# Kernel tuning notes

Measured on AMD Instinct MI355X. Metric: run time of the kernel, lower is better.

The kernel has to match this reference:

```python
import jax, jax.numpy as jnp
import numpy as np

EPS = 1e-5
NUM_HEADS = 8

def _inorm(x):
    # InstanceNorm1d (affine=False): normalize over last (length) axis per (B, C)
    m = x.mean(axis=-1, keepdims=True)
    v = x.var(axis=-1, keepdims=True)  # biased variance, as torch instance norm
    return (x - m) * jax.lax.rsqrt(v + EPS)

def setup_inputs() -> dict:
    key = jax.random.key(0)
    ks = jax.random.split(key, 12)
    B, Nl, HW = 4, 1024, 4096
    Cl, Cv, Ck, Cval, Cout = 512, 512, 256, 256, 256
    w = lambda k, shape: (jax.random.normal(k, shape, jnp.float32) * 0.02)
    return {
        "l": jax.random.normal(ks[0], (B, Nl, Cl), jnp.float32),
        "x": jax.random.normal(ks[1], (B, HW, Cv), jnp.float32),
        "Wq": w(ks[2], (Ck, Cl)),   "bq": w(ks[3], (Ck,)),
        "Wk": w(ks[4], (Ck, Cv)),   "bk": w(ks[5], (Ck,)),
        "Wv": w(ks[6], (Cval, Cv)), "bv": w(ks[7], (Cval,)),
        "Ww": w(ks[8], (Cout, Cval)), "bw": w(ks[9], (Cout,)),
    }

def reference(l, x, Wq, bq, Wk, bk, Wv, bv, Ww, bw):
    H = NUM_HEADS
    Ck = Wq.shape[0]
    Cv = Wv.shape[0]
    dk, dv = Ck // H, Cv // H
    B, Nl, _ = l.shape
    HW = x.shape[1]

    # 1x1 Conv1d == per-position linear
    q = jnp.einsum('blc,kc->blk', l, Wq) + bq                     # [B, Nl, Ck]
    k = jnp.einsum('bnc,kc->bkn', x, Wk) + bk[None, :, None]      # [B, Ck, HW]
    k = _inorm(k)                                                  # InstanceNorm over HW
    v = jnp.einsum('bnc,kc->bkn', x, Wv) + bv[None, :, None]      # [B, Cv, HW]

    q = q.reshape(B, Nl, H, dk).transpose(0, 2, 1, 3)             # [B, H, Nl, dk]
    k = k.reshape(B, H, dk, HW)                                   # [B, H, dk, HW]
    v = v.reshape(B, H, dv, HW)                                   # [B, H, dv, HW]

    sim = jnp.einsum('bhld,bhdn->bhln', q, k) * (Ck ** -0.5)      # [B, H, Nl, HW]
    att = jax.nn.softmax(sim, axis=-1)
    out = jnp.einsum('bhln,bhdn->bhld', att, v)                   # [B, H, Nl, dv]

    out = out.transpose(0, 2, 1, 3).reshape(B, Nl, Cv)            # [B, Nl, Cv]
    out = jnp.einsum('blc,oc->bol', out, Ww) + bw[None, :, None]  # [B, Cout, Nl]
    out = _inorm(out)                                              # InstanceNorm over Nl
    return out.transpose(0, 2, 1)                                  # [B, Nl, Cout]
```

## Files before the change

### kernel.cpp

```cpp
#include <hip/hip_runtime.h>

constexpr int Bn = 4, NL = 1024, HWn = 4096, NH = 8;

typedef __attribute__((ext_vector_type(8))) short bf16x8;
typedef __attribute__((ext_vector_type(4))) float f32x4;
#define MFMA16 __builtin_amdgcn_mfma_f32_16x16x32_bf16

extern "C" __device__ float __ocml_native_exp2_f32(float);

__device__ __forceinline__ float b2f(unsigned short u) {
  union { unsigned int i; float f; } x; x.i = ((unsigned int)u) << 16; return x.f;
}
__device__ __forceinline__ unsigned short f2b(float f) {
  union { float f; unsigned int i; } x; x.f = f;
  unsigned int r = x.i + 0x7fffu + ((x.i >> 16) & 1u);
  return (unsigned short)(r >> 16);
}

__device__ __forceinline__ void async_load16(const unsigned short* g, unsigned short* l) {
  __builtin_amdgcn_global_load_lds(
      (const __attribute__((address_space(1))) unsigned int*)g,
      (__attribute__((address_space(3))) unsigned int*)l, 16, 0, 0);
}

__global__ __launch_bounds__(256) void convall(const float* __restrict__ x,
    const float* __restrict__ l,
    const float* __restrict__ Wk, const float* __restrict__ Wv,
    const float* __restrict__ Wq, const float* __restrict__ Ww,
    unsigned short* __restrict__ xbf, unsigned short* __restrict__ lbf,
    unsigned short* __restrict__ wkb, unsigned short* __restrict__ wvb,
    unsigned short* __restrict__ wqb,
    unsigned short* __restrict__ wwh, unsigned short* __restrict__ wwl,
    float* __restrict__ Fz)
{
  const int id = blockIdx.x, tid = threadIdx.x;
  if (id < 8192) {
    int i = (id * 256 + tid) * 4;
    float4 v = *(const float4*)(x + i);
    ushort4 o; o.x = f2b(v.x); o.y = f2b(v.y); o.z = f2b(v.z); o.w = f2b(v.w);
    *(ushort4*)(xbf + i) = o;
  } else if (id < 10240) {
    int i = ((id - 8192) * 256 + tid) * 4;
    float4 v = *(const float4*)(l + i);
    ushort4 o; o.x = f2b(v.x); o.y = f2b(v.y); o.z = f2b(v.z); o.w = f2b(v.w);
    *(ushort4*)(lbf + i) = o;
  } else if (id < 10752) {
    int sub = id - 10240;
    int y = sub >> 7, bx = sub & 127;
    int i = (bx * 256 + tid) * 4;
    if (y == 3) {
      if (i >= 65536) return;
      float4 v = *(const float4*)(Ww + i);
      ushort4 hi, lo;
      hi.x = f2b(v.x); lo.x = f2b(v.x - b2f(hi.x));
      hi.y = f2b(v.y); lo.y = f2b(v.y - b2f(hi.y));
      hi.z = f2b(v.z); lo.z = f2b(v.z - b2f(hi.z));
      hi.w = f2b(v.w); lo.w = f2b(v.w - b2f(hi.w));
      *(ushort4*)(wwh + i) = hi;
      *(ushort4*)(wwl + i) = lo;
      return;
    }
    const float* src = y == 0 ? Wk : (y == 1 ? Wv : Wq);
    unsigned short* dst = y == 0 ? wkb : (y == 1 ? wvb : wqb);
    float4 v = *(const float4*)(src + i);
    ushort4 o; o.x = f2b(v.x); o.y = f2b(v.y); o.z = f2b(v.z); o.w = f2b(v.w);
    *(ushort4*)(dst + i) = o;
  } else {
    int i = (id - 10752) * 1024 + tid * 4;
    *(float4*)(Fz + i) = (float4){0.f, 0.f, 0.f, 0.f};
  }
}

__global__ __launch_bounds__(256, 3) void gemm128(
    const unsigned short* __restrict__ xbf, const unsigned short* __restrict__ lbf,
    const unsigned short* __restrict__ wkb, const unsigned short* __restrict__ wvb,
    const unsigned short* __restrict__ wqb,
    const float* __restrict__ bk, const float* __restrict__ bv, const float* __restrict__ bq,
    unsigned short* __restrict__ khb, unsigned short* __restrict__ vfrag,
    unsigned short* __restrict__ qbuf,
    float* __restrict__ ksum, float* __restrict__ kss, float* __restrict__ vcs)
{
  __shared__ unsigned short As[2][4096];
  __shared__ unsigned short Bs[2][4096];
  const int id = blockIdx.x;
  const int mode = id < 256 ? 0 : (id < 512 ? 1 : 2);
  const int local = id - (mode == 0 ? 0 : (mode == 1 ? 256 : 512));
  const int rb = local >> 1, cb = local & 1;
  const int m0 = rb * 128, n0 = cb * 128;
  const unsigned short* A = (mode == 2) ? lbf : xbf;
  const unsigned short* W = (mode == 0) ? wkb : (mode == 1 ? wvb : wqb);
  const float* bias = (mode == 0) ? bk : (mode == 1 ? bv : bq);

  const int tid = threadIdx.x, w = tid >> 6, lane = tid & 63;
  const int quad = lane >> 4, l15 = lane & 15;
  const int wr = w >> 1, wc = w & 1;

  const int p0 = tid, p1 = tid + 256;
  const int am0 = p0 >> 2, ak0 = (p0 & 3) * 8;
  const int am1 = p1 >> 2, ak1 = (p1 & 3) * 8;

  f32x4 acc[4][4];
#pragma unroll
  for (int i = 0; i < 4; ++i)
#pragma unroll
    for (int j = 0; j < 4; ++j) acc[i][j] = (f32x4){0.f, 0.f, 0.f, 0.f};

  async_load16(A + (size_t)(m0 + am0) * 512 + ak0, &As[0][p0 * 8]);
  async_load16(A + (size_t)(m0 + am1) * 512 + ak1, &As[0][p1 * 8]);
  async_load16(W + (size_t)(n0 + am0) * 512 + ak0, &Bs[0][p0 * 8]);
  async_load16(W + (size_t)(n0 + am1) * 512 + ak1, &Bs[0][p1 * 8]);

  for (int kt = 0; kt < 16; ++kt) {
    const int cur = kt & 1;
    __syncthreads();
    if (kt < 15) {
      int k0 = (kt + 1) * 32;
      async_load16(A + (size_t)(m0 + am0) * 512 + k0 + ak0, &As[cur ^ 1][p0 * 8]);
      async_load16(A + (size_t)(m0 + am1) * 512 + k0 + ak1, &As[cur ^ 1][p1 * 8]);
      async_load16(W + (size_t)(n0 + am0) * 512 + k0 + ak0, &Bs[cur ^ 1][p0 * 8]);
      async_load16(W + (size_t)(n0 + am1) * 512 + k0 + ak1, &Bs[cur ^ 1][p1 * 8]);
    }
    bf16x8 af[4], bf[4];
#pragma unroll
    for (int fr = 0; fr < 4; ++fr)
      af[fr] = *(const bf16x8*)&As[cur][(wr * 64 + fr * 16 + l15) * 32 + quad * 8];
#pragma unroll
    for (int fc = 0; fc < 4; ++fc)
      bf[fc] = *(const bf16x8*)&Bs[cur][(wc * 64 + fc * 16 + l15) * 32 + quad * 8];
#pragma unroll
    for (int fr = 0; fr < 4; ++fr)
#pragma unroll
      for (int fc = 0; fc < 4; ++fc)
        acc[fr][fc] = MFMA16(af[fr], bf[fc], acc[fr][fc], 0, 0, 0);
  }

  float bb[4];
#pragma unroll
  for (int fc = 0; fc < 4; ++fc) bb[fc] = bias[n0 + wc * 64 + fc * 16 + l15];

  if (mode != 2) {
    const int b = m0 >> 12;
    const int seg = (m0 & 4095) >> 9;
#pragma unroll
    for (int fc = 0; fc < 4; ++fc) {
      float s = 0.f, ssq = 0.f;
#pragma unroll
      for (int fr = 0; fr < 4; ++fr)
#pragma unroll
        for (int r = 0; r < 4; ++r) {
          float v = acc[fr][fc][r] + bb[fc];
          s += v; ssq += v * v;
        }
      s += __shfl_xor(s, 16); s += __shfl_xor(s, 32);
      if (mode == 0) {
        ssq += __shfl_xor(ssq, 16); ssq += __shfl_xor(ssq, 32);
        if (quad == 0) {
          int col = n0 + wc * 64 + fc * 16 + l15;
          atomicAdd(&ksum[b * 256 + col], s);
          atomicAdd(&kss[b * 256 + col], ssq);
        }
      } else if (quad == 0) {
        int col = n0 + wc * 64 + fc * 16 + l15;
        atomicAdd(&vcs[seg * 1024 + b * 256 + col], s);
      }
    }
  }

  if (mode == 1) {
    const int b = m0 >> 12;
    const int seg64 = ((m0 & 4095) >> 6) + wr;
#pragma unroll
    for (int fc = 0; fc < 4; ++fc) {
      int col = n0 + wc * 64 + fc * 16 + l15;
      int h = col >> 5, d = col & 31;
      int dvt = d >> 4, ll = d & 15;
      size_t base = (size_t)((b * 8 + h) * 64 + seg64) * 2048 + dvt * 512;
#pragma unroll
      for (int fr = 0; fr < 4; ++fr) {
#pragma unroll
        for (int r = 0; r < 4; ++r) {
          int kappa = 4 * (quad * 4 + r) + fr;
          int kh2 = kappa >> 5, lq = (kappa >> 3) & 3, j = kappa & 7;
          vfrag[base + kh2 * 1024 + (lq * 16 + ll) * 8 + j] = f2b(acc[fr][fc][r] + bb[fc]);
        }
      }
    }
  } else {
    unsigned short* dst = (mode == 0) ? khb : qbuf;
#pragma unroll
    for (int fr = 0; fr < 4; ++fr) {
#pragma unroll
      for (int fc = 0; fc < 4; ++fc) {
        int col = n0 + wc * 64 + fc * 16 + l15;
#pragma unroll
        for (int r = 0; r < 4; ++r) {
          int row = m0 + wr * 64 + fr * 16 + quad * 4 + r;
          unsigned short val = f2b(acc[fr][fc][r] + bb[fc]);
          if (mode == 2) {
            dst[(size_t)row * 256 + col] = val;
          } else {
            int b = row >> 12, n = row & 4095, h = col >> 5, d = col & 31;
            dst[((size_t)(b * 8 + h) * 4096 + n) * 32 + d] = val;
          }
        }
      }
    }
  }
}

__global__ __launch_bounds__(256, 4) void attn10(const unsigned short* __restrict__ qbuf,
    const unsigned short* __restrict__ khb, const unsigned short* __restrict__ vfrag,
    const float* __restrict__ ksum, const float* __restrict__ kss,
    const float* __restrict__ vcs,
    float* __restrict__ po, float* __restrict__ pd)
{
  const int bh = blockIdx.x, b = bh >> 3, h = bh & 7;
  const int lsuper = blockIdx.y, quarter = blockIdx.z;
  const int tid = threadIdx.x, w = tid >> 6, lane = tid & 63;
  const int quad = lane >> 4, l15 = lane & 15;

  __shared__ unsigned short ps[4][2][16][64];

  bf16x8 qa[2];
  {
    float fold[8];
    const int ch = bh * 32 + quad * 8;
#pragma unroll
    for (int j = 0; j < 8; ++j) {
      float m = ksum[ch + j] * (1.f / 4096.f);
      float var = kss[ch + j] * (1.f / 4096.f) - m * m;
      fold[j] = rsqrtf(var + 1e-5f) * (0.0625f * 1.44269504f);
    }
#pragma unroll
    for (int lf = 0; lf < 2; ++lf) {
      int l = lsuper * 128 + w * 32 + lf * 16 + l15;
      bf16x8 qr = *(const bf16x8*)(qbuf + ((size_t)(b * NL + l)) * 256 + h * 32 + quad * 8);
      const unsigned short* qq = (const unsigned short*)&qr;
      unsigned short tmp[8];
#pragma unroll
      for (int j = 0; j < 8; ++j) tmp[j] = f2b(b2f(qq[j]) * fold[j]);
      qa[lf] = *(const bf16x8*)tmp;
    }
  }

  float drow[2][4];
  f32x4 acc[2][2];
#pragma unroll
  for (int lf = 0; lf < 2; ++lf) {
#pragma unroll
    for (int r = 0; r < 4; ++r) drow[lf][r] = 0.f;
    acc[lf][0] = (f32x4){0.f,0.f,0.f,0.f};
    acc[lf][1] = (f32x4){0.f,0.f,0.f,0.f};
  }

  const unsigned short* kl = khb + (size_t)bh * 131072 + (size_t)quarter * 32768
                             + l15 * 32 + quad * 8;
  const unsigned short* vl = vfrag + (size_t)bh * 131072 + (size_t)quarter * 32768
                             + lane * 8;

  unsigned short* psw = &ps[w][0][0][0];
  const unsigned rdswz = (unsigned)((l15 & 7) << 4);

  for (int c = 0; c < 16; ++c) {
    bf16x8 kb[4], vb[4];
#pragma unroll
    for (int t = 0; t < 4; ++t)
      kb[t] = *(const bf16x8*)(kl + c * 2048 + t * 512);
#pragma unroll
    for (int i = 0; i < 4; ++i)
      vb[i] = *(const bf16x8*)(vl + c * 2048 + i * 512);

    const f32x4 z = (f32x4){0.f,0.f,0.f,0.f};
#pragma unroll
    for (int lf = 0; lf < 2; ++lf) {
      f32x4 sv[4];
      __builtin_amdgcn_s_setprio(1);
#pragma unroll
      for (int t = 0; t < 4; ++t) sv[t] = MFMA16(qa[lf], kb[t], z, 0, 0, 0);
      __builtin_amdgcn_s_setprio(0);
#pragma unroll
      for (int r = 0; r < 4; ++r) {
        float x0 = __ocml_native_exp2_f32(sv[0][r]);
        float x1 = __ocml_native_exp2_f32(sv[1][r]);
        float x2 = __ocml_native_exp2_f32(sv[2][r]);
        float x3 = __ocml_native_exp2_f32(sv[3][r]);
        drow[lf][r] += (x0 + x1) + (x2 + x3);
        unsigned pk0, pk1;
        asm("v_cvt_pk_bf16_f32 %0, %1, %2" : "=v"(pk0) : "v"(x0 - 1.0f), "v"(x1 - 1.0f));
        asm("v_cvt_pk_bf16_f32 %0, %1, %2" : "=v"(pk1) : "v"(x2 - 1.0f), "v"(x3 - 1.0f));
        const int row = quad * 4 + r;
        unsigned off = (unsigned)((l15 * 8) ^ ((row & 7) << 4));
        uint2 pk; pk.x = pk0; pk.y = pk1;
        *(uint2*)((char*)(psw + lf * 1024 + row * 64) + off) = pk;
      }
      asm volatile("s_waitcnt lgkmcnt(0)" ::: "memory");
      __builtin_amdgcn_s_setprio(1);
#pragma unroll
      for (int kh2 = 0; kh2 < 2; ++kh2) {
        unsigned off = (unsigned)((kh2 * 64 + quad * 16) ^ rdswz);
        bf16x8 pa = *(const bf16x8*)((const char*)(psw + lf * 1024 + l15 * 64) + off);
        acc[lf][0] = MFMA16(pa, vb[kh2 * 2 + 0], acc[lf][0], 0, 0, 0);
        acc[lf][1] = MFMA16(pa, vb[kh2 * 2 + 1], acc[lf][1], 0, 0, 0);
      }
      __builtin_amdgcn_s_setprio(0);
    }
  }

  const float* vc0 = vcs + (quarter * 2) * 1024 + bh * 32;
  const float* vc1 = vc0 + 1024;
  float cs0 = vc0[l15] + vc1[l15];
  float cs1 = vc0[16 + l15] + vc1[16 + l15];
#pragma unroll
  for (int lf = 0; lf < 2; ++lf)
#pragma unroll
    for (int r = 0; r < 4; ++r) {
      acc[lf][0][r] += cs0;
      acc[lf][1][r] += cs1;
    }

  const size_t PDo = (size_t)quarter * 32768 + (size_t)bh * 1024;
#pragma unroll
  for (int lf = 0; lf < 2; ++lf) {
#pragma unroll
    for (int r = 0; r < 4; ++r) {
      float sv = drow[lf][r];
      sv += __shfl_xor(sv, 1, 16);
      sv += __shfl_xor(sv, 2, 16);
      sv += __shfl_xor(sv, 4, 16);
      sv += __shfl_xor(sv, 8, 16);
      int l = lsuper * 128 + w * 32 + lf * 16 + quad * 4 + r;
      float2 val; val.x = acc[lf][0][r]; val.y = acc[lf][1][r];
      *(float2*)(po + (PDo + l) * 32 + l15 * 2) = val;
      if (l15 == 0) pd[PDo + l] = sv;
    }
  }
}

__global__ __launch_bounds__(256) void combine4(const float* __restrict__ po,
    const float* __restrict__ pd, unsigned short* __restrict__ aoh,
    unsigned short* __restrict__ aol)
{
  int gid = blockIdx.x * 256 + threadIdx.x;
  int dv = gid & 31, l = (gid >> 5) & (NL - 1), h = (gid >> 15) & 7, b = gid >> 18;
  int c = ((dv & 15) << 1) | (dv >> 4);
  size_t r = ((size_t)(b * 8 + h)) * 1024 + l;
  float d = 0.f, o = 0.f;
#pragma unroll
  for (int q = 0; q < 4; ++q) {
    size_t rr = (size_t)q * 32768 + r;
    d += pd[rr];
    o += po[rr * 32 + c];
  }
  o = o / d;
  unsigned short hi = f2b(o);
  size_t idx = ((size_t)(b * NL) + l) * 256 + h * 32 + dv;
  aoh[idx] = hi;
  aol[idx] = f2b(o - b2f(hi));
}

__global__ __launch_bounds__(256) void gemm_proj(
    const unsigned short* __restrict__ aoh, const unsigned short* __restrict__ aol,
    const unsigned short* __restrict__ wwh, const unsigned short* __restrict__ wwl,
    const float* __restrict__ bw, float* __restrict__ pj,
    float* __restrict__ psum, float* __restrict__ psq)
{
  __shared__ unsigned short As[64 * 32];
  __shared__ unsigned short Bs[64 * 32];
  const int bm = blockIdx.x * 64, bn = blockIdx.y * 64;
  const int tid = threadIdx.x, w = tid >> 6, lane = tid & 63;
  const int quad = lane >> 4, l15 = lane & 15;
  const int wr = w >> 1, wc = w & 1;
  const int arow = tid >> 2, apiece = (tid & 3) * 8;

  f32x4 acc[2][2];
#pragma unroll
  for (int i = 0; i < 2; ++i)
#pragma unroll
    for (int j = 0; j < 2; ++j) acc[i][j] = (f32x4){0.f, 0.f, 0.f, 0.f};

  for (int pair = 0; pair < 3; ++pair) {
    const unsigned short* A = (pair == 1) ? aol : aoh;
    const unsigned short* Bm = (pair == 2) ? wwl : wwh;
    for (int kt = 0; kt < 8; ++kt) {
      int k0 = kt * 32;
      __syncthreads();
      *(bf16x8*)&As[tid * 8] = *(const bf16x8*)(A + (size_t)(bm + arow) * 256 + k0 + apiece);
      *(bf16x8*)&Bs[tid * 8] = *(const bf16x8*)(Bm + (size_t)(bn + arow) * 256 + k0 + apiece);
      __syncthreads();
      bf16x8 af[2], bf[2];
#pragma unroll
      for (int fr = 0; fr < 2; ++fr)
        af[fr] = *(const bf16x8*)&As[(wr * 32 + fr * 16 + l15) * 32 + quad * 8];
#pragma unroll
      for (int fc = 0; fc < 2; ++fc)
        bf[fc] = *(const bf16x8*)&Bs[(wc * 32 + fc * 16 + l15) * 32 + quad * 8];
#pragma unroll
      for (int fr = 0; fr < 2; ++fr)
#pragma unroll
        for (int fc = 0; fc < 2; ++fc)
          acc[fr][fc] = MFMA16(af[fr], bf[fc], acc[fr][fc], 0, 0, 0);
    }
  }

  const int b = bm >> 10;
#pragma unroll
  for (int fr = 0; fr < 2; ++fr)
#pragma unroll
    for (int fc = 0; fc < 2; ++fc) {
      int col = bn + wc * 32 + fc * 16 + l15;
      float bb = bw[col];
      float s = 0.f, ssq = 0.f;
#pragma unroll
      for (int r = 0; r < 4; ++r) {
        int row = bm + wr * 32 + fr * 16 + quad * 4 + r;
        float v = acc[fr][fc][r] + bb;
        pj[(size_t)row * 256 + col] = v;
        s += v; ssq += v * v;
      }
      s += __shfl_xor(s, 16); s += __shfl_xor(s, 32);
      ssq += __shfl_xor(ssq, 16); ssq += __shfl_xor(ssq, 32);
      if (quad == 0) {
        atomicAdd(&psum[b * 256 + col], s);
        atomicAdd(&psq[b * 256 + col], ssq);
      }
    }
}

__global__ __launch_bounds__(256) void final_out(const float* __restrict__ proj,
    const float* __restrict__ psum, const float* __restrict__ psq,
    float* __restrict__ out)
{
  const int b = blockIdx.x, o = threadIdx.x;
  const int l1 = blockIdx.y * 16;
  const float m = psum[b * 256 + o] * (1.f / 1024.f);
  const float r = rsqrtf(psq[b * 256 + o] * (1.f / 1024.f) - m * m + 1e-5f);
  for (int i = 0; i < 16; ++i) {
    size_t idx = ((size_t)(b * NL + l1 + i)) * 256 + o;
    out[idx] = (proj[idx] - m) * r;
  }
}

extern "C" void kernel_launch(void* const* d_in, const int* in_sizes, int n_in,
                              void* d_out, int out_size, void* d_ws, size_t ws_size,
                              hipStream_t stream)
{
  const float* l  = (const float*)d_in[0];
  const float* x  = (const float*)d_in[1];
  const float* Wq = (const float*)d_in[2];
  const float* bq = (const float*)d_in[3];
  const float* Wk = (const float*)d_in[4];
  const float* bk = (const float*)d_in[5];
  const float* Wv = (const float*)d_in[6];
  const float* bv = (const float*)d_in[7];
  const float* Ww = (const float*)d_in[8];
  const float* bw = (const float*)d_in[9];
  float* out = (float*)d_out;

  unsigned short* up = (unsigned short*)d_ws;
  unsigned short* xbf   = up;
  unsigned short* lbf   = xbf   + 8388608;
  unsigned short* wkb   = lbf   + 2097152;
  unsigned short* wvb   = wkb   + 131072;
  unsigned short* wqb   = wvb   + 131072;
  unsigned short* qbuf  = wqb   + 131072;
  unsigned short* khb   = qbuf  + 1048576;
  unsigned short* vhb   = khb   + 4194304;
  unsigned short* vfrag = vhb   + 4194304;
  unsigned short* aoh   = vfrag + 4194304;
  unsigned short* aol   = aoh   + 1048576;
  unsigned short* wwh   = aol   + 1048576;
  unsigned short* wwl   = wwh   + 65536;
  float* F     = (float*)((char*)d_ws + 53477376);
  float* ksum  = F;
  float* kss   = F + 1024;
  float* vcs   = F + 2048;
  float* psum  = F + 10240;
  float* psq   = F + 11264;
  float* po    = F + 15360;
  float* pd    = po + 4194304;
  float* pj    = po;

  dim3 blk(256);
  convall<<<10764, blk, 0, stream>>>(x, l, Wk, Wv, Wq, Ww, xbf, lbf,
                                     wkb, wvb, wqb, wwh, wwl, F);
  gemm128<<<576, blk, 0, stream>>>(xbf, lbf, wkb, wvb, wqb, bk, bv, bq,
                                   khb, vfrag, qbuf, ksum, kss, vcs);
  attn10<<<dim3(32, 8, 4), blk, 0, stream>>>(qbuf, khb, vfrag, ksum, kss, vcs, po, pd);
  combine4<<<4096, blk, 0, stream>>>(po, pd, aoh, aol);
  gemm_proj<<<dim3(64, 4), blk, 0, stream>>>(aoh, aol, wwh, wwl, bw, pj, psum, psq);
  final_out<<<dim3(4, 64), blk, 0, stream>>>(pj, psum, psq, out);
}
```

Measured before the change: 172.6 us.

## Fuse attention split-K combine into attention kernel, stage V-fragment stores, pipeline proj GEMM

The attention kernel no longer splits the HW axis into four quarters. Each block now walks all 64 key chunks for 16 query rows per wave and normalizes its output in place, writing the hi/lo bf16 split directly. This removes the combine4 kernel and the round trip of partial outputs and denominators through global memory, at the cost of fewer query rows per wave and a smaller grid. Separately, the QKV GEMM stages its V-fragment output through LDS so global stores become 16-byte coalesced, and the projection GEMM gains double-buffered async LDS loads.

```diff
diff --git a/kernel.cpp b/kernel.cpp
--- a/kernel.cpp
+++ b/kernel.cpp
@@ -80,8 +80,9 @@
     unsigned short* __restrict__ qbuf,
     float* __restrict__ ksum, float* __restrict__ kss, float* __restrict__ vcs)
 {
-  __shared__ unsigned short As[2][4096];
-  __shared__ unsigned short Bs[2][4096];
+  __shared__ unsigned short sh[16384];
+  unsigned short* As0 = sh;
+  unsigned short* Bs0 = sh + 8192;
   const int id = blockIdx.x;
   const int mode = id < 256 ? 0 : (id < 512 ? 1 : 2);
   const int local = id - (mode == 0 ? 0 : (mode == 1 ? 256 : 512));
@@ -105,28 +106,29 @@
 #pragma unroll
     for (int j = 0; j < 4; ++j) acc[i][j] = (f32x4){0.f, 0.f, 0.f, 0.f};
 
-  async_load16(A + (size_t)(m0 + am0) * 512 + ak0, &As[0][p0 * 8]);
-  async_load16(A + (size_t)(m0 + am1) * 512 + ak1, &As[0][p1 * 8]);
-  async_load16(W + (size_t)(n0 + am0) * 512 + ak0, &Bs[0][p0 * 8]);
-  async_load16(W + (size_t)(n0 + am1) * 512 + ak1, &Bs[0][p1 * 8]);
+  async_load16(A + (size_t)(m0 + am0) * 512 + ak0, &As0[p0 * 8]);
+  async_load16(A + (size_t)(m0 + am1) * 512 + ak1, &As0[p1 * 8]);
+  async_load16(W + (size_t)(n0 + am0) * 512 + ak0, &Bs0[p0 * 8]);
+  async_load16(W + (size_t)(n0 + am1) * 512 + ak1, &Bs0[p1 * 8]);
 
   for (int kt = 0; kt < 16; ++kt) {
     const int cur = kt & 1;
     __syncthreads();
     if (kt < 15) {
       int k0 = (kt + 1) * 32;
-      async_load16(A + (size_t)(m0 + am0) * 512 + k0 + ak0, &As[cur ^ 1][p0 * 8]);
-      async_load16(A + (size_t)(m0 + am1) * 512 + k0 + ak1, &As[cur ^ 1][p1 * 8]);
-      async_load16(W + (size_t)(n0 + am0) * 512 + k0 + ak0, &Bs[cur ^ 1][p0 * 8]);
-      async_load16(W + (size_t)(n0 + am1) * 512 + k0 + ak1, &Bs[cur ^ 1][p1 * 8]);
+      int nx = (cur ^ 1) * 4096;
+      async_load16(A + (size_t)(m0 + am0) * 512 + k0 + ak0, &As0[nx + p0 * 8]);
+      async_load16(A + (size_t)(m0 + am1) * 512 + k0 + ak1, &As0[nx + p1 * 8]);
+      async_load16(W + (size_t)(n0 + am0) * 512 + k0 + ak0, &Bs0[nx + p0 * 8]);
+      async_load16(W + (size_t)(n0 + am1) * 512 + k0 + ak1, &Bs0[nx + p1 * 8]);
     }
     bf16x8 af[4], bf[4];
 #pragma unroll
     for (int fr = 0; fr < 4; ++fr)
-      af[fr] = *(const bf16x8*)&As[cur][(wr * 64 + fr * 16 + l15) * 32 + quad * 8];
+      af[fr] = *(const bf16x8*)&As0[cur * 4096 + (wr * 64 + fr * 16 + l15) * 32 + quad * 8];
 #pragma unroll
     for (int fc = 0; fc < 4; ++fc)
-      bf[fc] = *(const bf16x8*)&Bs[cur][(wc * 64 + fc * 16 + l15) * 32 + quad * 8];
+      bf[fc] = *(const bf16x8*)&Bs0[cur * 4096 + (wc * 64 + fc * 16 + l15) * 32 + quad * 8];
 #pragma unroll
     for (int fr = 0; fr < 4; ++fr)
 #pragma unroll
@@ -167,23 +169,31 @@
   }
 
   if (mode == 1) {
-    const int b = m0 >> 12;
-    const int seg64 = ((m0 & 4095) >> 6) + wr;
+    __syncthreads();
 #pragma unroll
     for (int fc = 0; fc < 4; ++fc) {
-      int col = n0 + wc * 64 + fc * 16 + l15;
-      int h = col >> 5, d = col & 31;
-      int dvt = d >> 4, ll = d & 15;
-      size_t base = (size_t)((b * 8 + h) * 64 + seg64) * 2048 + dvt * 512;
+      const int ls = wr * 4 + wc * 2 + ((fc * 16 + l15) >> 5);
+      const int dvt = fc & 1;
 #pragma unroll
       for (int fr = 0; fr < 4; ++fr) {
 #pragma unroll
         for (int r = 0; r < 4; ++r) {
           int kappa = 4 * (quad * 4 + r) + fr;
           int kh2 = kappa >> 5, lq = (kappa >> 3) & 3, j = kappa & 7;
-          vfrag[base + kh2 * 1024 + (lq * 16 + ll) * 8 + j] = f2b(acc[fr][fc][r] + bb[fc]);
+          sh[ls * 2048 + kh2 * 1024 + dvt * 512 + lq * 128 + l15 * 8 + j] =
+              f2b(acc[fr][fc][r] + bb[fc]);
         }
       }
+    }
+    __syncthreads();
+    const int b2 = m0 >> 12, h0 = cb * 4, seg64b = (m0 & 4095) >> 6;
+#pragma unroll
+    for (int i = 0; i < 8; ++i) {
+      int p = i * 256 + tid;
+      int ls = p >> 8, off8 = (p & 255) * 8;
+      int dh = ls & 3, wr2 = ls >> 2;
+      size_t dst = ((size_t)((b2 * 8 + h0 + dh) * 64) + seg64b + wr2) * 2048 + off8;
+      *(bf16x8*)(vfrag + dst) = *(const bf16x8*)&sh[ls * 2048 + off8];
     }
   } else {
     unsigned short* dst = (mode == 0) ? khb : qbuf;
@@ -208,20 +218,20 @@
   }
 }
 
-__global__ __launch_bounds__(256, 4) void attn10(const unsigned short* __restrict__ qbuf,
+__global__ __launch_bounds__(256, 2) void attn11(const unsigned short* __restrict__ qbuf,
     const unsigned short* __restrict__ khb, const unsigned short* __restrict__ vfrag,
     const float* __restrict__ ksum, const float* __restrict__ kss,
     const float* __restrict__ vcs,
-    float* __restrict__ po, float* __restrict__ pd)
+    unsigned short* __restrict__ aoh, unsigned short* __restrict__ aol)
 {
   const int bh = blockIdx.x, b = bh >> 3, h = bh & 7;
-  const int lsuper = blockIdx.y, quarter = blockIdx.z;
+  const int lsuper = blockIdx.y;
   const int tid = threadIdx.x, w = tid >> 6, lane = tid & 63;
   const int quad = lane >> 4, l15 = lane & 15;
 
-  __shared__ unsigned short ps[4][2][16][64];
-
-  bf16x8 qa[2];
+  __shared__ unsigned short ps[4][16][64];
+
+  bf16x8 qa;
   {
     float fold[8];
     const int ch = bh * 32 + quad * 8;
@@ -231,37 +241,27 @@
       float var = kss[ch + j] * (1.f / 4096.f) - m * m;
       fold[j] = rsqrtf(var + 1e-5f) * (0.0625f * 1.44269504f);
     }
-#pragma unroll
-    for (int lf = 0; lf < 2; ++lf) {
-      int l = lsuper * 128 + w * 32 + lf * 16 + l15;
-      bf16x8 qr = *(const bf16x8*)(qbuf + ((size_t)(b * NL + l)) * 256 + h * 32 + quad * 8);
-      const unsigned short* qq = (const unsigned short*)&qr;
-      unsigned short tmp[8];
-#pragma unroll
-      for (int j = 0; j < 8; ++j) tmp[j] = f2b(b2f(qq[j]) * fold[j]);
-      qa[lf] = *(const bf16x8*)tmp;
-    }
-  }
-
-  float drow[2][4];
-  f32x4 acc[2][2];
-#pragma unroll
-  for (int lf = 0; lf < 2; ++lf) {
-#pragma unroll
-    for (int r = 0; r < 4; ++r) drow[lf][r] = 0.f;
-    acc[lf][0] = (f32x4){0.f,0.f,0.f,0.f};
-    acc[lf][1] = (f32x4){0.f,0.f,0.f,0.f};
-  }
-
-  const unsigned short* kl = khb + (size_t)bh * 131072 + (size_t)quarter * 32768
-                             + l15 * 32 + quad * 8;
-  const unsigned short* vl = vfrag + (size_t)bh * 131072 + (size_t)quarter * 32768
-                             + lane * 8;
-
-  unsigned short* psw = &ps[w][0][0][0];
+    int l = lsuper * 64 + w * 16 + l15;
+    bf16x8 qr = *(const bf16x8*)(qbuf + ((size_t)(b * NL + l)) * 256 + h * 32 + quad * 8);
+    const unsigned short* qq = (const unsigned short*)&qr;
+    unsigned short tmp[8];
+#pragma unroll
+    for (int j = 0; j < 8; ++j) tmp[j] = f2b(b2f(qq[j]) * fold[j]);
+    qa = *(const bf16x8*)tmp;
+  }
+
+  float drow[4] = {0.f, 0.f, 0.f, 0.f};
+  f32x4 acc[2];
+  acc[0] = (f32x4){0.f,0.f,0.f,0.f};
+  acc[1] = (f32x4){0.f,0.f,0.f,0.f};
+
+  const unsigned short* kl = khb + (size_t)bh * 131072 + l15 * 32 + quad * 8;
+  const unsigned short* vl = vfrag + (size_t)bh * 131072 + lane * 8;
+
+  unsigned short* psw = &ps[w][0][0];
   const unsigned rdswz = (unsigned)((l15 & 7) << 4);
 
-  for (int c = 0; c < 16; ++c) {
+  for (int c = 0; c < 64; ++c) {
     bf16x8 kb[4], vb[4];
 #pragma unroll
     for (int t = 0; t < 4; ++t)
@@ -271,91 +271,63 @@
       vb[i] = *(const bf16x8*)(vl + c * 2048 + i * 512);
 
     const f32x4 z = (f32x4){0.f,0.f,0.f,0.f};
-#pragma unroll
-    for (int lf = 0; lf < 2; ++lf) {
-      f32x4 sv[4];
-      __builtin_amdgcn_s_setprio(1);
-#pragma unroll
-      for (int t = 0; t < 4; ++t) sv[t] = MFMA16(qa[lf], kb[t], z, 0, 0, 0);
-      __builtin_amdgcn_s_setprio(0);
-#pragma unroll
-      for (int r = 0; r < 4; ++r) {
-        float x0 = __ocml_native_exp2_f32(sv[0][r]);
-        float x1 = __ocml_native_exp2_f32(sv[1][r]);
-        float x2 = __ocml_native_exp2_f32(sv[2][r]);
-        float x3 = __ocml_native_exp2_f32(sv[3][r]);
-        drow[lf][r] += (x0 + x1) + (x2 + x3);
-        unsigned pk0, pk1;
-        asm("v_cvt_pk_bf16_f32 %0, %1, %2" : "=v"(pk0) : "v"(x0 - 1.0f), "v"(x1 - 1.0f));
-        asm("v_cvt_pk_bf16_f32 %0, %1, %2" : "=v"(pk1) : "v"(x2 - 1.0f), "v"(x3 - 1.0f));
-        const int row = quad * 4 + r;
-        unsigned off = (unsigned)((l15 * 8) ^ ((row & 7) << 4));
-        uint2 pk; pk.x = pk0; pk.y = pk1;
-        *(uint2*)((char*)(psw + lf * 1024 + row * 64) + off) = pk;
-      }
-      asm volatile("s_waitcnt lgkmcnt(0)" ::: "memory");
-      __builtin_amdgcn_s_setprio(1);
-#pragma unroll
-      for (int kh2 = 0; kh2 < 2; ++kh2) {
-        unsigned off = (unsigned)((kh2 * 64 + quad * 16) ^ rdswz);
-        bf16x8 pa = *(const bf16x8*)((const char*)(psw + lf * 1024 + l15 * 64) + off);
-        acc[lf][0] = MFMA16(pa, vb[kh2 * 2 + 0], acc[lf][0], 0, 0, 0);
-        acc[lf][1] = MFMA16(pa, vb[kh2 * 2 + 1], acc[lf][1], 0, 0, 0);
-      }
-      __builtin_amdgcn_s_setprio(0);
-    }
-  }
-
-  const float* vc0 = vcs + (quarter * 2) * 1024 + bh * 32;
-  const float* vc1 = vc0 + 1024;
-  float cs0 = vc0[l15] + vc1[l15];
-  float cs1 = vc0[16 + l15] + vc1[16 + l15];
-#pragma unroll
-  for (int lf = 0; lf < 2; ++lf)
+    f32x4 sv[4];
+    __builtin_amdgcn_s_setprio(1);
+#pragma unroll
+    for (int t = 0; t < 4; ++t) sv[t] = MFMA16(qa, kb[t], z, 0, 0, 0);
+    __builtin_amdgcn_s_setprio(0);
 #pragma unroll
     for (int r = 0; r < 4; ++r) {
-      acc[lf][0][r] += cs0;
-      acc[lf][1][r] += cs1;
-    }
-
-  const size_t PDo = (size_t)quarter * 32768 + (size_t)bh * 1024;
-#pragma unroll
-  for (int lf = 0; lf < 2; ++lf) {
-#pragma unroll
-    for (int r = 0; r < 4; ++r) {
-      float sv = drow[lf][r];
-      sv += __shfl_xor(sv, 1, 16);
-      sv += __shfl_xor(sv, 2, 16);
-      sv += __shfl_xor(sv, 4, 16);
-      sv += __shfl_xor(sv, 8, 16);
-      int l = lsuper * 128 + w * 32 + lf * 16 + quad * 4 + r;
-      float2 val; val.x = acc[lf][0][r]; val.y = acc[lf][1][r];
-      *(float2*)(po + (PDo + l) * 32 + l15 * 2) = val;
-      if (l15 == 0) pd[PDo + l] = sv;
-    }
-  }
-}
-
-__global__ __launch_bounds__(256) void combine4(const float* __restrict__ po,
-    const float* __restrict__ pd, unsigned short* __restrict__ aoh,
-    unsigned short* __restrict__ aol)
-{
-  int gid = blockIdx.x * 256 + threadIdx.x;
-  int dv = gid & 31, l = (gid >> 5) & (NL - 1), h = (gid >> 15) & 7, b = gid >> 18;
-  int c = ((dv & 15) << 1) | (dv >> 4);
-  size_t r = ((size_t)(b * 8 + h)) * 1024 + l;
-  float d = 0.f, o = 0.f;
-#pragma unroll
-  for (int q = 0; q < 4; ++q) {
-    size_t rr = (size_t)q * 32768 + r;
-    d += pd[rr];
-    o += po[rr * 32 + c];
-  }
-  o = o / d;
-  unsigned short hi = f2b(o);
-  size_t idx = ((size_t)(b * NL) + l) * 256 + h * 32 + dv;
-  aoh[idx] = hi;
-  aol[idx] = f2b(o - b2f(hi));
+      float x0 = __ocml_native_exp2_f32(sv[0][r]);
+      float x1 = __ocml_native_exp2_f32(sv[1][r]);
+      float x2 = __ocml_native_exp2_f32(sv[2][r]);
+      float x3 = __ocml_native_exp2_f32(sv[3][r]);
+      drow[r] += (x0 + x1) + (x2 + x3);
+      unsigned pk0, pk1;
+      asm("v_cvt_pk_bf16_f32 %0, %1, %2" : "=v"(pk0) : "v"(x0 - 1.0f), "v"(x1 - 1.0f));
+      asm("v_cvt_pk_bf16_f32 %0, %1, %2" : "=v"(pk1) : "v"(x2 - 1.0f), "v"(x3 - 1.0f));
+      const int row = quad * 4 + r;
+      unsigned off = (unsigned)((l15 * 8) ^ ((row & 7) << 4));
+      uint2 pk; pk.x = pk0; pk.y = pk1;
+      *(uint2*)((char*)(psw + row * 64) + off) = pk;
+    }
+    asm volatile("s_waitcnt lgkmcnt(0)" ::: "memory");
+    __builtin_amdgcn_s_setprio(1);
+#pragma unroll
+    for (int kh2 = 0; kh2 < 2; ++kh2) {
+      unsigned off = (unsigned)((kh2 * 64 + quad * 16) ^ rdswz);
+      bf16x8 pa = *(const bf16x8*)((const char*)(psw + l15 * 64) + off);
+      acc[0] = MFMA16(pa, vb[kh2 * 2 + 0], acc[0], 0, 0, 0);
+      acc[1] = MFMA16(pa, vb[kh2 * 2 + 1], acc[1], 0, 0, 0);
+    }
+    __builtin_amdgcn_s_setprio(0);
+  }
+
+  float cs0 = 0.f, cs1 = 0.f;
+#pragma unroll
+  for (int s = 0; s < 8; ++s) {
+    cs0 += vcs[s * 1024 + bh * 32 + l15];
+    cs1 += vcs[s * 1024 + bh * 32 + 16 + l15];
+  }
+
+#pragma unroll
+  for (int r = 0; r < 4; ++r) {
+    float sv = drow[r];
+    sv += __shfl_xor(sv, 1, 16);
+    sv += __shfl_xor(sv, 2, 16);
+    sv += __shfl_xor(sv, 4, 16);
+    sv += __shfl_xor(sv, 8, 16);
+    int l = lsuper * 64 + w * 16 + quad * 4 + r;
+    size_t idx = ((size_t)(b * NL) + l) * 256 + h * 32;
+    float o0 = (acc[0][r] + cs0) / sv;
+    float o1 = (acc[1][r] + cs1) / sv;
+    unsigned short h0s = f2b(o0);
+    unsigned short h1s = f2b(o1);
+    aoh[idx + l15]      = h0s;
+    aol[idx + l15]      = f2b(o0 - b2f(h0s));
+    aoh[idx + 16 + l15] = h1s;
+    aol[idx + 16 + l15] = f2b(o1 - b2f(h1s));
+  }
 }
 
 __global__ __launch_bounds__(256) void gemm_proj(
@@ -364,8 +336,8 @@
     const float* __restrict__ bw, float* __restrict__ pj,
     float* __restrict__ psum, float* __restrict__ psq)
 {
-  __shared__ unsigned short As[64 * 32];
-  __shared__ unsigned short Bs[64 * 32];
+  __shared__ unsigned short As[2][2048];
+  __shared__ unsigned short Bs[2][2048];
   const int bm = blockIdx.x * 64, bn = blockIdx.y * 64;
   const int tid = threadIdx.x, w = tid >> 6, lane = tid & 63;
   const int quad = lane >> 4, l15 = lane & 15;
@@ -378,28 +350,33 @@
 #pragma unroll
     for (int j = 0; j < 2; ++j) acc[i][j] = (f32x4){0.f, 0.f, 0.f, 0.f};
 
-  for (int pair = 0; pair < 3; ++pair) {
-    const unsigned short* A = (pair == 1) ? aol : aoh;
-    const unsigned short* Bm = (pair == 2) ? wwl : wwh;
-    for (int kt = 0; kt < 8; ++kt) {
-      int k0 = kt * 32;
-      __syncthreads();
-      *(bf16x8*)&As[tid * 8] = *(const bf16x8*)(A + (size_t)(bm + arow) * 256 + k0 + apiece);
-      *(bf16x8*)&Bs[tid * 8] = *(const bf16x8*)(Bm + (size_t)(bn + arow) * 256 + k0 + apiece);
-      __syncthreads();
-      bf16x8 af[2], bf[2];
-#pragma unroll
-      for (int fr = 0; fr < 2; ++fr)
-        af[fr] = *(const bf16x8*)&As[(wr * 32 + fr * 16 + l15) * 32 + quad * 8];
+  async_load16(aoh + (size_t)(bm + arow) * 256 + apiece, &As[0][tid * 8]);
+  async_load16(wwh + (size_t)(bn + arow) * 256 + apiece, &Bs[0][tid * 8]);
+
+  for (int it = 0; it < 24; ++it) {
+    const int cur = it & 1;
+    __syncthreads();
+    if (it < 23) {
+      int nx = it + 1;
+      int p = nx >> 3;
+      const unsigned short* An = (p == 1) ? aol : aoh;
+      const unsigned short* Bm = (p == 2) ? wwl : wwh;
+      int k0 = (nx & 7) * 32;
+      async_load16(An + (size_t)(bm + arow) * 256 + k0 + apiece, &As[cur ^ 1][tid * 8]);
+      async_load16(Bm + (size_t)(bn + arow) * 256 + k0 + apiece, &Bs[cur ^ 1][tid * 8]);
+    }
+    bf16x8 af[2], bf[2];
+#pragma unroll
+    for (int fr = 0; fr < 2; ++fr)
+      af[fr] = *(const bf16x8*)&As[cur][(wr * 32 + fr * 16 + l15) * 32 + quad * 8];
+#pragma unroll
+    for (int fc = 0; fc < 2; ++fc)
+      bf[fc] = *(const bf16x8*)&Bs[cur][(wc * 32 + fc * 16 + l15) * 32 + quad * 8];
+#pragma unroll
+    for (int fr = 0; fr < 2; ++fr)
 #pragma unroll
       for (int fc = 0; fc < 2; ++fc)
-        bf[fc] = *(const bf16x8*)&Bs[(wc * 32 + fc * 16 + l15) * 32 + quad * 8];
-#pragma unroll
-      for (int fr = 0; fr < 2; ++fr)
-#pragma unroll
-        for (int fc = 0; fc < 2; ++fc)
-          acc[fr][fc] = MFMA16(af[fr], bf[fc], acc[fr][fc], 0, 0, 0);
-    }
+        acc[fr][fc] = MFMA16(af[fr], bf[fc], acc[fr][fc], 0, 0, 0);
   }
 
   const int b = bm >> 10;
@@ -476,17 +453,14 @@
   float* vcs   = F + 2048;
   float* psum  = F + 10240;
   float* psq   = F + 11264;
-  float* po    = F + 15360;
-  float* pd    = po + 4194304;
-  float* pj    = po;
+  float* pj    = F + 15360;
 
   dim3 blk(256);
   convall<<<10764, blk, 0, stream>>>(x, l, Wk, Wv, Wq, Ww, xbf, lbf,
                                      wkb, wvb, wqb, wwh, wwl, F);
   gemm128<<<576, blk, 0, stream>>>(xbf, lbf, wkb, wvb, wqb, bk, bv, bq,
                                    khb, vfrag, qbuf, ksum, kss, vcs);
-  attn10<<<dim3(32, 8, 4), blk, 0, stream>>>(qbuf, khb, vfrag, ksum, kss, vcs, po, pd);
-  combine4<<<4096, blk, 0, stream>>>(po, pd, aoh, aol);
+  attn11<<<dim3(32, 16), blk, 0, stream>>>(qbuf, khb, vfrag, ksum, kss, vcs, aoh, aol);
   gemm_proj<<<dim3(64, 4), blk, 0, stream>>>(aoh, aol, wwh, wwl, bw, pj, psum, psq);
   final_out<<<dim3(4, 64), blk, 0, stream>>>(pj, psum, psq, out);
 }
```

New measurement: 177.0 us. +2.5%, slower.
